# Performance work log

Measured on AMD Instinct MI355X. Metric: run time of the kernel, lower is better.

Reference implementation:

```python
import jax, jax.numpy as jnp
import numpy as np
from jax import lax

B = 512
P_KEEP = 0.5  # base dropout keep probability (p=0.5)


def conv(x, w, b, pad):
    y = lax.conv_general_dilated(x, w, (1, 1), [(pad, pad), (pad, pad)],
                                 dimension_numbers=('NCHW', 'OIHW', 'NCHW'))
    return y + b[None, :, None, None]


def maxpool3s2(x):
    return lax.reduce_window(x, -jnp.inf, lax.max, (1, 1, 3, 3), (1, 1, 2, 2), 'VALID')


def eb_linear(p_out, a, W):
    # Excitation backprop through a linear layer (bias ignored).
    # p_out: [B, out] marginal winning probs at layer output
    # a:     [B, in]  (non-negative) activations at layer input
    # W:     [out, in]
    Wp = jnp.maximum(W, 0.0)
    z = a @ Wp.T                              # [B, out]
    s = jnp.where(z > 0, p_out / z, 0.0)      # [B, out]
    return a * (s @ Wp)                       # [B, in]


def setup_inputs() -> dict:
    key = jax.random.key(0)
    ks = jax.random.split(key, 16)

    def w(k, shape, fan_in):
        return (jax.random.normal(k, shape, jnp.float32) / np.sqrt(fan_in)).astype(jnp.float32)

    return {
        'x': jax.random.normal(ks[0], (B, 3, 32, 32), jnp.float32),
        'noise': jax.random.uniform(ks[1], (B, 2048), jnp.float32),
        'conv1_w': w(ks[2], (96, 3, 5, 5), 3 * 25),
        'conv1_b': jnp.zeros((96,), jnp.float32),
        'conv2_w': w(ks[3], (128, 96, 5, 5), 96 * 25),
        'conv2_b': jnp.zeros((128,), jnp.float32),
        'conv3_w': w(ks[4], (256, 128, 5, 5), 128 * 25),
        'conv3_b': jnp.zeros((256,), jnp.float32),
        'fc1_w': w(ks[5], (2048, 1024), 1024),
        'fc1_b': jnp.zeros((2048,), jnp.float32),
        'fc2_w': w(ks[6], (2048, 2048), 2048),
        'fc2_b': jnp.zeros((2048,), jnp.float32),
        'fc3_w': w(ks[7], (10, 2048), 2048),
        'fc3_b': jnp.zeros((10,), jnp.float32),
        'label': jax.random.randint(ks[8], (B,), 0, 10),
    }


def reference(x, noise, conv1_w, conv1_b, conv2_w, conv2_b, conv3_w, conv3_b,
              fc1_w, fc1_b, fc2_w, fc2_b, fc3_w, fc3_b, label):
    h1 = maxpool3s2(jax.nn.relu(conv(x, conv1_w, conv1_b, 1)))   # [B,96,14,14]
    h2 = maxpool3s2(jax.nn.relu(conv(h1, conv2_w, conv2_b, 2)))  # [B,128,6,6]
    h3 = maxpool3s2(jax.nn.relu(conv(h2, conv3_w, conv3_b, 2)))  # [B,256,2,2]
    h4 = h3.reshape(h3.shape[0], -1)                             # [B,1024]
    h5 = jax.nn.relu(h4 @ fc1_w.T + fc1_b)                       # [B,2048]

    # --- Excitation backprop through latterModel (fc2 -> relu -> fc3), batched ---
    h6_eb = jax.nn.relu(h5 @ fc2_w.T + fc2_b)                    # [B,2048]
    p_out = jax.nn.one_hot(label, 10, dtype=h5.dtype)            # [B,10]
    p_h6 = eb_linear(p_out, h6_eb, fc3_w)                        # [B,2048]
    pebs = eb_linear(p_h6, h5, fc2_w)                            # [B,2048]

    # --- Excitation Dropout mask ---
    N = pebs.shape[1]
    num = (1.0 - P_KEEP) * (N - 1) * pebs
    retain_p = 1.0 - num / (num + P_KEEP * (1.0 - pebs))         # [B,2048]
    mask = (noise < retain_p).astype(h5.dtype)
    h_ed = jnp.where(retain_p > 0, h5 * mask / retain_p, 0.0)

    h6 = jax.nn.relu(h_ed @ fc2_w.T + fc2_b)                     # [B,2048]
    return h6 @ fc3_w.T + fc3_b                                  # [B,10]
```

## Files before the change

### kernel.cpp

```cpp
#include <hip/hip_runtime.h>
#include <hip/hip_bf16.h>


typedef __attribute__((ext_vector_type(8))) short bf16x8;
typedef __attribute__((ext_vector_type(4))) float f32x4;

__device__ __forceinline__ void split_bf16(float x, ushort& h, ushort& l) {
    __hip_bfloat16 bh = __float2bfloat16(x);
    float fh = __bfloat162float(bh);
    __hip_bfloat16 bl = __float2bfloat16(x - fh);
    h = *(ushort*)&bh;
    l = *(ushort*)&bl;
}

__device__ __forceinline__ void split3_bf16(float x, ushort& a, ushort& b,
                                            ushort& c) {
    __hip_bfloat16 ba = __float2bfloat16(x);
    float fa = __bfloat162float(ba);
    float r = x - fa;
    __hip_bfloat16 bb = __float2bfloat16(r);
    float fb = __bfloat162float(bb);
    __hip_bfloat16 bc = __float2bfloat16(r - fb);
    a = *(ushort*)&ba;
    b = *(ushort*)&bb;
    c = *(ushort*)&bc;
}

__device__ __forceinline__ void gld_lds16(const void* g, void* l) {
    __builtin_amdgcn_global_load_lds(
        (const __attribute__((address_space(1))) unsigned int*)g,
        (__attribute__((address_space(3))) unsigned int*)l, 16, 0, 0);
}

__global__ void zero_k(float4* __restrict__ p, int n4) {
    int idx = blockIdx.x * 256 + threadIdx.x;
    int stride = gridDim.x * 256;
    float4 z = {0.f, 0.f, 0.f, 0.f};
    for (int i = idx; i < n4; i += stride) p[i] = z;
}

__global__ void transw_k(const float* __restrict__ in, float* __restrict__ out,
                         int OC, int K) {
    int idx = blockIdx.x * 256 + threadIdx.x;
    if (idx >= OC * K) return;
    int oc = idx / K, k = idx % K;
    out[k * OC + oc] = in[idx];
}

__global__ void splitw_k(const float* __restrict__ in, ushort* __restrict__ hi,
                         ushort* __restrict__ lo, int OC, int IC) {
    int idx = blockIdx.x * 256 + threadIdx.x;
    if (idx >= OC * IC * 25) return;
    int oc = idx / (IC * 25);
    int r = idx % (IC * 25);
    int ic = r / 25, tap = r % 25;
    float v = in[idx];
    ushort h, l;
    split_bf16(v, h, l);
    size_t k = (size_t)oc * IC * 25 + tap * IC + ic;
    hi[k] = h;
    lo[k] = l;
}

__global__ void splitw3_k(const float* __restrict__ in, ushort* __restrict__ out,
                          int off, int total) {
    int idx = blockIdx.x * 256 + threadIdx.x;
    if (idx >= total) return;
    ushort a, b, c;
    split3_bf16(in[idx], a, b, c);
    out[idx] = a;
    out[idx + off] = b;
    out[idx + 2 * off] = c;
}

__global__ __launch_bounds__(256) void splitw3t_relu_k(
        const float* __restrict__ in, ushort* __restrict__ out, int off) {
    __shared__ float tile[64][65];
    const int bx = blockIdx.x & 31, by = blockIdx.x >> 5;
    const int j = threadIdx.x & 63, i0 = threadIdx.x >> 6;
    for (int i = i0; i < 64; i += 4)
        tile[i][j] = in[(size_t)(by * 64 + i) * 2048 + bx * 64 + j];
    __syncthreads();
    for (int r = i0; r < 64; r += 4) {
        float x = fmaxf(tile[j][r], 0.f);
        ushort a, b, c;
        split3_bf16(x, a, b, c);
        size_t o = (size_t)(bx * 64 + r) * 2048 + by * 64 + j;
        out[o] = a;
        out[o + off] = b;
        out[o + 2 * off] = c;
    }
}

__global__ __launch_bounds__(256) void conv1_v3(
        const float* __restrict__ x, const float* __restrict__ w1t,
        const float* __restrict__ b1, ushort* __restrict__ h1hi,
        ushort* __restrict__ h1lo) {
    __shared__ float simg[3 * 34 * 34];
    __shared__ float c1s[8][904];
    const int b = blockIdx.x, oc0 = blockIdx.y * 8, t = threadIdx.x;

    for (int i = t; i < 3 * 34 * 34; i += 256) simg[i] = 0.f;
    __syncthreads();
    for (int i = t; i < 3072; i += 256) {
        int ic = i >> 10, r = (i >> 5) & 31, c = i & 31;
        simg[ic * 1156 + (r + 1) * 34 + (c + 1)] = x[(size_t)b * 3072 + i];
    }
    __syncthreads();

    int base[4];
    bool valid[4];
#pragma unroll
    for (int j = 0; j < 4; j++) {
        int p = t + j * 256;
        valid[j] = p < 900;
        int oh = p / 30, ow = p % 30;
        base[j] = valid[j] ? oh * 34 + ow : 0;
    }

    float acc[4][8];
#pragma unroll
    for (int j = 0; j < 4; j++)
#pragma unroll
        for (int u = 0; u < 8; u++) acc[j][u] = 0.f;

#pragma unroll 1
    for (int ic = 0; ic < 3; ic++) {
        const int icb = ic * 1156;
#pragma unroll 1
        for (int kh = 0; kh < 5; kh++) {
#pragma unroll
            for (int kw = 0; kw < 5; kw++) {
                const float4* wr =
                    (const float4*)&w1t[(ic * 25 + kh * 5 + kw) * 96 + oc0];
                float4 w0 = wr[0], w1v = wr[1];
#pragma unroll
                for (int j = 0; j < 4; j++) {
                    float v = simg[icb + base[j] + kh * 34 + kw];
#pragma unroll
                    for (int u = 0; u < 4; u++) {
                        acc[j][u] = fmaf((&w0.x)[u], v, acc[j][u]);
                        acc[j][u + 4] = fmaf((&w1v.x)[u], v, acc[j][u + 4]);
                    }
                }
            }
        }
    }
#pragma unroll
    for (int j = 0; j < 4; j++)
        if (valid[j]) {
            int p = t + j * 256;
#pragma unroll
            for (int u = 0; u < 8; u++) c1s[u][p] = acc[j][u];
        }
    __syncthreads();
    if (t < 196) {
        const int ph = t / 14, pw = t % 14;
        ushort hv[8], lv[8];
#pragma unroll
        for (int u = 0; u < 8; u++) {
            float m = c1s[u][(2 * ph) * 30 + 2 * pw];
#pragma unroll
            for (int q = 1; q < 9; q++) {
                int dy = q / 3, dx = q % 3;
                m = fmaxf(m, c1s[u][(2 * ph + dy) * 30 + 2 * pw + dx]);
            }
            float o = fmaxf(m + b1[oc0 + u], 0.f);
            split_bf16(o, hv[u], lv[u]);
        }
        size_t ob = (((size_t)b * 18 + ph + 2) * 18 + pw + 2) * 96 + oc0;
        *(bf16x8*)&h1hi[ob] = *(bf16x8*)&hv[0];
        *(bf16x8*)&h1lo[ob] = *(bf16x8*)&lv[0];
    }
}

template <int IC, int H, int W, int OH, int OW, int OC, int NM>
__global__ __launch_bounds__(512, 2) void convmfma8_k(
        const ushort* __restrict__ ah, int aoff,
        const ushort* __restrict__ wh, int boff,
        const float* __restrict__ bias, float* __restrict__ C) {
    constexpr int K = 25 * IC;
    constexpr int G = NM * (OC / 128);
    __shared__ ushort At[2][128 * 64];
    __shared__ ushort Bt[2][128 * 64];
    const int t = threadIdx.x;
    const int lane = t & 63, wv = t >> 6;
    const int id = blockIdx.x;
    const int id2 = (id & 7) * (G >> 3) + (id >> 3);
    const int n0 = (id2 / NM) * 128;
    const int m0 = (id2 % NM) * 128;
    const int wm = (wv >> 1) * 32;
    const int wn = (wv & 1) * 64;

    const int srow = lane >> 3;
    const int slot = lane & 7;
    const int part = slot ^ srow;
    const bool hiA = part < 4;
    const int pk = (part & 3) * 8;

    int arb[2];
#pragma unroll
    for (int rr = 0; rr < 2; rr++) {
        int r = wv * 16 + rr * 8 + srow;
        int m = m0 + r;
        int b = m / (OH * OW), pxy = m % (OH * OW);
        int oh = pxy / OW, ow = pxy % OW;
        arb[rr] = ((b * H + oh) * W + ow) * IC + pk;
    }
    const ushort* __restrict__ aptr = ah + (hiA ? 0 : aoff);
    size_t brb[2];
#pragma unroll
    for (int rr = 0; rr < 2; rr++) {
        int r = wv * 16 + rr * 8 + srow;
        brb[rr] = (size_t)(n0 + r) * K + pk;
    }
    const ushort* __restrict__ bptr = wh + (hiA ? 0 : boff);

    f32x4 acc[2][4];
#pragma unroll
    for (int i = 0; i < 2; i++)
#pragma unroll
        for (int j = 0; j < 4; j++) acc[i][j] = (f32x4)(0.f);

    const int q = lane >> 4;
    const int fr = lane & 15;

    auto stage = [&](int buf, int k0s) {
        const int tap = k0s / IC;
        const int koff = ((tap / 5) * W + (tap % 5)) * IC + (k0s - tap * IC);
#pragma unroll
        for (int rr = 0; rr < 2; rr++)
            gld_lds16(aptr + arb[rr] + koff, &At[buf][(wv * 16 + rr * 8) * 64]);
#pragma unroll
        for (int rr = 0; rr < 2; rr++)
            gld_lds16(bptr + brb[rr] + k0s, &Bt[buf][(wv * 16 + rr * 8) * 64]);
    };

    stage(0, 0);
    __syncthreads();

    int cur = 0;
#pragma unroll 1
    for (int k0 = 0; k0 < K; k0 += 32) {
        bf16x8 afh[2], afl[2], bfh[4], bfl[4];
#pragma unroll
        for (int i = 0; i < 2; i++) {
            int row = wm + fr + i * 16;
            afh[i] = *(const bf16x8*)&At[cur][row * 64 + ((q ^ (row & 7)) << 3)];
            afl[i] = *(const bf16x8*)&At[cur][row * 64 + (((4 | q) ^ (row & 7)) << 3)];
        }
#pragma unroll
        for (int j = 0; j < 4; j++) {
            int row = wn + fr + j * 16;
            bfh[j] = *(const bf16x8*)&Bt[cur][row * 64 + ((q ^ (row & 7)) << 3)];
            bfl[j] = *(const bf16x8*)&Bt[cur][row * 64 + (((4 | q) ^ (row & 7)) << 3)];
        }
        const int nxt = k0 + 32;
        if (nxt < K) stage(cur ^ 1, nxt);

        __builtin_amdgcn_s_setprio(1);
#pragma unroll
        for (int i = 0; i < 2; i++)
#pragma unroll
            for (int j = 0; j < 4; j++) {
                acc[i][j] = __builtin_amdgcn_mfma_f32_16x16x32_bf16(
                    afh[i], bfh[j], acc[i][j], 0, 0, 0);
                acc[i][j] = __builtin_amdgcn_mfma_f32_16x16x32_bf16(
                    afh[i], bfl[j], acc[i][j], 0, 0, 0);
                acc[i][j] = __builtin_amdgcn_mfma_f32_16x16x32_bf16(
                    afl[i], bfh[j], acc[i][j], 0, 0, 0);
            }
        __builtin_amdgcn_s_setprio(0);
        __syncthreads();
        cur ^= 1;
    }

    const int crow0 = (lane >> 4) * 4;
    const int ccol = lane & 15;
#pragma unroll
    for (int i = 0; i < 2; i++) {
        int gm = m0 + wm + i * 16 + crow0;
#pragma unroll
        for (int j = 0; j < 4; j++) {
            int gn = n0 + wn + j * 16 + ccol;
            float bb = bias[gn];
#pragma unroll
            for (int r = 0; r < 4; r++)
                C[(size_t)(gm + r) * OC + gn] = acc[i][j][r] + bb;
        }
    }
}

template <int IC, int H, int W, int OH, int OW, int OC, int NM>
__global__ __launch_bounds__(256, 3) void convmfma9_k(
        const ushort* __restrict__ ah, int aoff,
        const ushort* __restrict__ wh, int boff,
        const float* __restrict__ bias, float* __restrict__ C) {
    constexpr int K = 25 * IC;
    constexpr int G = NM * (OC / 128);
    __shared__ ushort At[2][64 * 64];
    __shared__ ushort Bt[128 * 64];
    const int t = threadIdx.x;
    const int lane = t & 63, wv = t >> 6;
    const int id = blockIdx.x;
    const int id2 = (id & 7) * (G >> 3) + (id >> 3);
    const int n0 = (id2 / NM) * 128;
    const int m0 = (id2 % NM) * 64;
    const int wm = (wv >> 1) * 32;
    const int wn = (wv & 1) * 64;

    const int srow = lane >> 3;
    const int slot = lane & 7;
    const int part = slot ^ srow;
    const bool hiA = part < 4;
    const int pk = (part & 3) * 8;

    int arb[2];
#pragma unroll
    for (int rr = 0; rr < 2; rr++) {
        int r = wv * 16 + rr * 8 + srow;
        int m = m0 + r;
        int b = m / (OH * OW), pxy = m % (OH * OW);
        int oh = pxy / OW, ow = pxy % OW;
        arb[rr] = ((b * H + oh) * W + ow) * IC + pk;
    }
    const ushort* __restrict__ aptr = ah + (hiA ? 0 : aoff);
    size_t brb[4];
#pragma unroll
    for (int rr = 0; rr < 4; rr++) {
        int r = wv * 32 + rr * 8 + srow;
        brb[rr] = (size_t)(n0 + r) * K + pk;
    }
    const ushort* __restrict__ bptr = wh + (hiA ? 0 : boff);

    f32x4 acc[2][4];
#pragma unroll
    for (int i = 0; i < 2; i++)
#pragma unroll
        for (int j = 0; j < 4; j++) acc[i][j] = (f32x4)(0.f);

    const int q = lane >> 4;
    const int fr = lane & 15;

    auto stageA = [&](int buf, int k0s) {
        const int tap = k0s / IC;
        const int koff = ((tap / 5) * W + (tap % 5)) * IC + (k0s - tap * IC);
#pragma unroll
        for (int rr = 0; rr < 2; rr++)
            gld_lds16(aptr + arb[rr] + koff, &At[buf][(wv * 16 + rr * 8) * 64]);
    };
    auto stageB = [&](int k0s) {
#pragma unroll
        for (int rr = 0; rr < 4; rr++)
            gld_lds16(bptr + brb[rr] + k0s, &Bt[(wv * 32 + rr * 8) * 64]);
    };

    stageA(0, 0);
    stageB(0);
    __syncthreads();

    int cur = 0;
#pragma unroll 1
    for (int k0 = 0; k0 < K; k0 += 32) {
        bf16x8 bfh[4], bfl[4];
#pragma unroll
        for (int j = 0; j < 4; j++) {
            int row = wn + fr + j * 16;
            bfh[j] = *(const bf16x8*)&Bt[row * 64 + ((q ^ (row & 7)) << 3)];
            bfl[j] = *(const bf16x8*)&Bt[row * 64 + (((4 | q) ^ (row & 7)) << 3)];
        }
        __syncthreads();
        const int nxt = k0 + 32;
        if (nxt < K) {
            stageA(cur ^ 1, nxt);
            stageB(nxt);
        }
        bf16x8 afh[2], afl[2];
#pragma unroll
        for (int i = 0; i < 2; i++) {
            int row = wm + fr + i * 16;
            afh[i] = *(const bf16x8*)&At[cur][row * 64 + ((q ^ (row & 7)) << 3)];
            afl[i] = *(const bf16x8*)&At[cur][row * 64 + (((4 | q) ^ (row & 7)) << 3)];
        }
        __builtin_amdgcn_s_setprio(1);
#pragma unroll
        for (int i = 0; i < 2; i++)
#pragma unroll
            for (int j = 0; j < 4; j++) {
                acc[i][j] = __builtin_amdgcn_mfma_f32_16x16x32_bf16(
                    afh[i], bfh[j], acc[i][j], 0, 0, 0);
                acc[i][j] = __builtin_amdgcn_mfma_f32_16x16x32_bf16(
                    afh[i], bfl[j], acc[i][j], 0, 0, 0);
                acc[i][j] = __builtin_amdgcn_mfma_f32_16x16x32_bf16(
                    afl[i], bfh[j], acc[i][j], 0, 0, 0);
            }
        __builtin_amdgcn_s_setprio(0);
        __syncthreads();
        cur ^= 1;
    }

    const int crow0 = (lane >> 4) * 4;
    const int ccol = lane & 15;
#pragma unroll
    for (int i = 0; i < 2; i++) {
        int gm = m0 + wm + i * 16 + crow0;
#pragma unroll
        for (int j = 0; j < 4; j++) {
            int gn = n0 + wn + j * 16 + ccol;
            float bb = bias[gn];
#pragma unroll
            for (int r = 0; r < 4; r++)
                C[(size_t)(gm + r) * OC + gn] = acc[i][j][r] + bb;
        }
    }
}

__global__ void pool2_k(const float* __restrict__ in, ushort* __restrict__ ohi,
                        ushort* __restrict__ olo) {
    int idx = blockIdx.x * 256 + threadIdx.x;
    if (idx >= 512 * 36 * 128) return;
    int c = idx & 127;
    int tmp = idx >> 7;
    int pw = tmp % 6;
    int tmp2 = tmp / 6;
    int ph = tmp2 % 6;
    int b = tmp2 / 6;
    size_t base = (((size_t)b * 14 + 2 * ph) * 14 + 2 * pw) * 128 + c;
    float m = -3.4e38f;
#pragma unroll
    for (int dy = 0; dy < 3; dy++)
#pragma unroll
        for (int dx = 0; dx < 3; dx++)
            m = fmaxf(m, in[base + (dy * 14 + dx) * 128]);
    float v = fmaxf(m, 0.f);
    ushort h, l;
    split_bf16(v, h, l);
    size_t o = (((size_t)b * 10 + ph + 2) * 10 + pw + 2) * 128 + c;
    ohi[o] = h;
    olo[o] = l;
}

__global__ void pool3_k(const float* __restrict__ in, float* __restrict__ h3) {
    int idx = blockIdx.x * 256 + threadIdx.x;
    if (idx >= 512 * 4 * 256) return;
    int c = idx & 255;
    int pw = (idx >> 8) & 1;
    int ph = (idx >> 9) & 1;
    int b = idx >> 10;
    size_t base = (((size_t)b * 6 + 2 * ph) * 6 + 2 * pw) * 256 + c;
    float m = -3.4e38f;
#pragma unroll
    for (int dy = 0; dy < 3; dy++)
#pragma unroll
        for (int dx = 0; dx < 3; dx++)
            m = fmaxf(m, in[base + (dy * 6 + dx) * 256]);
    h3[(size_t)b * 1024 + c * 4 + ph * 2 + pw] = fmaxf(m, 0.f);
}

template <int BIAS, int RELUOUT, int DUAL>
__global__ __launch_bounds__(256, 4) void gemmfc_k(
        const float* __restrict__ A, const ushort* __restrict__ B3, int boff,
        const float* __restrict__ bias, float* __restrict__ C,
        float* __restrict__ C2, int K, int N) {
    __shared__ ushort Aa[32][44], Ab[32][44], Ac[32][44];
    __shared__ ushort Ba[64][44], Bb[64][44], Bc[64][44];
    const int t = threadIdx.x;
    const int n0 = blockIdx.x * 64;
    const int m0 = blockIdx.y * 32;
    const int lane = t & 63, wv = t >> 6;
    const int wm = (wv >> 1) * 16, wn = (wv & 1) * 32;
    const int fr = lane & 15, kp = (lane >> 4) * 8;

    f32x4 acc[2], acc2[DUAL ? 2 : 1];
#pragma unroll
    for (int j = 0; j < 2; j++) acc[j] = (f32x4)(0.f);
    if constexpr (DUAL) {
#pragma unroll
        for (int j = 0; j < 2; j++) acc2[j] = (f32x4)(0.f);
    }

    const int ar = t >> 2, ak = (t & 3) * 8;

    for (int k0 = 0; k0 < K; k0 += 32) {
        float4 a0, a1;
        if (t < 128) {
            a0 = *(const float4*)&A[(size_t)(m0 + ar) * K + k0 + ak];
            a1 = *(const float4*)&A[(size_t)(m0 + ar) * K + k0 + ak + 4];
        }
        size_t bidx = (size_t)(n0 + ar) * K + k0 + ak;
        bf16x8 b0 = *(const bf16x8*)&B3[bidx];
        bf16x8 b1 = *(const bf16x8*)&B3[bidx + boff];
        bf16x8 b2 = *(const bf16x8*)&B3[bidx + 2 * (size_t)boff];
        __syncthreads();
        if (t < 128) {
            ushort sa[8], sb[8], sc[8];
#pragma unroll
            for (int e = 0; e < 4; e++)
                split3_bf16((&a0.x)[e], sa[e], sb[e], sc[e]);
#pragma unroll
            for (int e = 0; e < 4; e++)
                split3_bf16((&a1.x)[e], sa[4 + e], sb[4 + e], sc[4 + e]);
            *(bf16x8*)&Aa[ar][ak] = *(bf16x8*)sa;
            *(bf16x8*)&Ab[ar][ak] = *(bf16x8*)sb;
            *(bf16x8*)&Ac[ar][ak] = *(bf16x8*)sc;
        }
        *(bf16x8*)&Ba[ar][ak] = b0;
        *(bf16x8*)&Bb[ar][ak] = b1;
        *(bf16x8*)&Bc[ar][ak] = b2;
        __syncthreads();

        bf16x8 fa = *(const bf16x8*)&Aa[wm + fr][kp];
        bf16x8 fb = *(const bf16x8*)&Ab[wm + fr][kp];
        bf16x8 fc = *(const bf16x8*)&Ac[wm + fr][kp];
#pragma unroll
        for (int j = 0; j < 2; j++) {
            int row = wn + j * 16 + fr;
            bf16x8 ga = *(const bf16x8*)&Ba[row][kp];
            bf16x8 gb = *(const bf16x8*)&Bb[row][kp];
            bf16x8 gc = *(const bf16x8*)&Bc[row][kp];
            acc[j] = __builtin_amdgcn_mfma_f32_16x16x32_bf16(fa, ga, acc[j], 0, 0, 0);
            acc[j] = __builtin_amdgcn_mfma_f32_16x16x32_bf16(fa, gb, acc[j], 0, 0, 0);
            acc[j] = __builtin_amdgcn_mfma_f32_16x16x32_bf16(fb, ga, acc[j], 0, 0, 0);
            acc[j] = __builtin_amdgcn_mfma_f32_16x16x32_bf16(fa, gc, acc[j], 0, 0, 0);
            acc[j] = __builtin_amdgcn_mfma_f32_16x16x32_bf16(fc, ga, acc[j], 0, 0, 0);
            acc[j] = __builtin_amdgcn_mfma_f32_16x16x32_bf16(fb, gb, acc[j], 0, 0, 0);
            if constexpr (DUAL) {
                bf16x8 msk = ga >> 15;
                bf16x8 ra = ga & ~msk;
                bf16x8 rb = gb & ~msk;
                bf16x8 rc = gc & ~msk;
                acc2[j] = __builtin_amdgcn_mfma_f32_16x16x32_bf16(fa, ra, acc2[j], 0, 0, 0);
                acc2[j] = __builtin_amdgcn_mfma_f32_16x16x32_bf16(fa, rb, acc2[j], 0, 0, 0);
                acc2[j] = __builtin_amdgcn_mfma_f32_16x16x32_bf16(fb, ra, acc2[j], 0, 0, 0);
                acc2[j] = __builtin_amdgcn_mfma_f32_16x16x32_bf16(fa, rc, acc2[j], 0, 0, 0);
                acc2[j] = __builtin_amdgcn_mfma_f32_16x16x32_bf16(fc, ra, acc2[j], 0, 0, 0);
                acc2[j] = __builtin_amdgcn_mfma_f32_16x16x32_bf16(fb, rb, acc2[j], 0, 0, 0);
            }
        }
    }

    const int gm0 = m0 + wm + (lane >> 4) * 4;
#pragma unroll
    for (int j = 0; j < 2; j++) {
        int gn = n0 + wn + j * 16 + fr;
        float bb = BIAS ? bias[gn] : 0.f;
#pragma unroll
        for (int r = 0; r < 4; r++) {
            float v = acc[j][r] + bb;
            if constexpr (RELUOUT) v = fmaxf(v, 0.f);
            C[(size_t)(gm0 + r) * N + gn] = v;
            if constexpr (DUAL) C2[(size_t)(gm0 + r) * N + gn] = acc2[j][r];
        }
    }
}

__global__ __launch_bounds__(256) void zlab_k(
        const float* __restrict__ h6eb, const float* __restrict__ w3,
        const int* __restrict__ label, float* __restrict__ zlab) {
    __shared__ float red[4];
    const int b = blockIdx.x, t = threadIdx.x;
    const int lab = label[b];
    const float4* hp = (const float4*)(h6eb + (size_t)b * 2048);
    const float4* wp = (const float4*)(w3 + (size_t)lab * 2048);
    float s = 0.f;
    for (int i = t; i < 512; i += 256) {
        float4 h = hp[i], w = wp[i];
        s += h.x * fmaxf(w.x, 0.f) + h.y * fmaxf(w.y, 0.f) +
             h.z * fmaxf(w.z, 0.f) + h.w * fmaxf(w.w, 0.f);
    }
#pragma unroll
    for (int off = 32; off > 0; off >>= 1) s += __shfl_down(s, off, 64);
    if ((t & 63) == 0) red[t >> 6] = s;
    __syncthreads();
    if (t == 0) zlab[b] = red[0] + red[1] + red[2] + red[3];
}

__global__ void s2_k(const float* __restrict__ h6eb, const float* __restrict__ z2,
                     const float* __restrict__ w3, const int* __restrict__ label,
                     const float* __restrict__ zlab, float* __restrict__ s2) {
    int idx = blockIdx.x * 256 + threadIdx.x;
    int b = idx >> 11, j = idx & 2047;
    float zl = zlab[b], zv = z2[idx];
    float v = 0.f;
    if (zl > 0.f && zv > 0.f) {
        float wp = fmaxf(w3[(size_t)label[b] * 2048 + j], 0.f);
        v = h6eb[idx] * wp / (zl * zv);
    }
    s2[idx] = v;
}

__global__ void edrop_k(const float* __restrict__ h5, const float* __restrict__ t,
                        const float* __restrict__ noise, float* __restrict__ hed) {
    int idx = blockIdx.x * 256 + threadIdx.x;
    float pe = h5[idx] * t[idx];
    float num = 1023.5f * pe;
    float retain = 1.f - num / (num + 0.5f * (1.f - pe));
    float m = (noise[idx] < retain) ? 1.f : 0.f;
    hed[idx] = (retain > 0.f) ? h5[idx] * m / retain : 0.f;
}

__global__ void fc3_out_k(const float* __restrict__ h6, const float* __restrict__ w,
                          const float* __restrict__ bias, float* __restrict__ out) {
    int idx = blockIdx.x * 256 + threadIdx.x;
    if (idx >= 5120) return;
    int b = idx / 10, c = idx % 10;
    const float4* hp = (const float4*)(h6 + (size_t)b * 2048);
    const float4* wp = (const float4*)(w + (size_t)c * 2048);
    float s = 0.f;
    for (int i = 0; i < 512; i++) {
        float4 h = hp[i], ww = wp[i];
        s += h.x * ww.x + h.y * ww.y + h.z * ww.z + h.w * ww.w;
    }
    out[idx] = s + bias[c];
}

extern "C" void kernel_launch(void* const* d_in, const int* in_sizes, int n_in,
                              void* d_out, int out_size, void* d_ws, size_t ws_size,
                              hipStream_t stream) {
    const float* x       = (const float*)d_in[0];
    const float* noise   = (const float*)d_in[1];
    const float* conv1_w = (const float*)d_in[2];
    const float* conv1_b = (const float*)d_in[3];
    const float* conv2_w = (const float*)d_in[4];
    const float* conv2_b = (const float*)d_in[5];
    const float* conv3_w = (const float*)d_in[6];
    const float* conv3_b = (const float*)d_in[7];
    const float* fc1_w   = (const float*)d_in[8];
    const float* fc1_b   = (const float*)d_in[9];
    const float* fc2_w   = (const float*)d_in[10];
    const float* fc2_b   = (const float*)d_in[11];
    const float* fc3_w   = (const float*)d_in[12];
    const float* fc3_b   = (const float*)d_in[13];
    const int*   label   = (const int*)d_in[14];
    float* out = (float*)d_out;

    const size_t N_H1 = (size_t)512 * 18 * 18 * 96;
    const size_t N_C2 = (size_t)512 * 14 * 14 * 128;
    const size_t N_H2 = (size_t)512 * 10 * 10 * 128;
    const size_t N_H3 = (size_t)512 * 1024;

    float* ws = (float*)d_ws;
    ushort* h1hi = (ushort*)ws;
    ushort* h1lo = h1hi + N_H1;
    float* c3 = ws;
    float* c2 = ws + N_H1;
    float* h5   = c2;
    float* h6eb = c2 + 1 * 1048576;
    float* z2   = c2 + 2 * 1048576;
    float* s2   = c2 + 3 * 1048576;
    float* tb   = c2 + 4 * 1048576;
    float* hed  = c2 + 5 * 1048576;
    float* h6   = c2 + 6 * 1048576;
    float* zlab = c2 + 7 * 1048576;
    ushort* h2hi = (ushort*)(ws + N_H1 + N_C2);
    ushort* h2lo = h2hi + N_H2;
    float* h3  = ws + N_H1 + N_C2 + N_H2;
    float* w1t = h3 + N_H3;
    ushort* w2sh = (ushort*)(w1t + 7200);
    ushort* w2sl = w2sh + 307200;
    ushort* w3sh = w2sl + 307200;
    ushort* w3sl = w3sh + 819200;
    ushort* w23  = w3sl + 819200;
    ushort* w2rt = w23 + 3 * 4194304;
    ushort* w13  = w2rt + 3 * 4194304;

    transw_k<<<(75 * 96 + 255) / 256, 256, 0, stream>>>(conv1_w, w1t, 96, 75);
    splitw_k<<<(307200 + 255) / 256, 256, 0, stream>>>(conv2_w, w2sh, w2sl, 128, 96);
    splitw_k<<<(819200 + 255) / 256, 256, 0, stream>>>(conv3_w, w3sh, w3sl, 256, 128);
    splitw3_k<<<16384, 256, 0, stream>>>(fc2_w, w23, 4194304, 4194304);
    splitw3t_relu_k<<<1024, 256, 0, stream>>>(fc2_w, w2rt, 4194304);
    splitw3_k<<<8192, 256, 0, stream>>>(fc1_w, w13, 2097152, 2097152);

    zero_k<<<2048, 256, 0, stream>>>((float4*)h1hi, (int)(N_H1 / 4));
    zero_k<<<2048, 256, 0, stream>>>((float4*)h2hi, (int)(N_H2 / 4));

    conv1_v3<<<dim3(512, 12), 256, 0, stream>>>(x, w1t, conv1_b, h1hi, h1lo);
    convmfma8_k<96, 18, 18, 14, 14, 128, 784><<<784, 512, 0, stream>>>(
        h1hi, (int)N_H1, w2sh, 307200, conv2_b, c2);
    pool2_k<<<(512 * 36 * 128 + 255) / 256, 256, 0, stream>>>(c2, h2hi, h2lo);
    convmfma9_k<128, 10, 10, 6, 6, 256, 288><<<576, 256, 0, stream>>>(
        h2hi, (int)N_H2, w3sh, 819200, conv3_b, c3);
    pool3_k<<<(512 * 4 * 256 + 255) / 256, 256, 0, stream>>>(c3, h3);

    gemmfc_k<1, 1, 0><<<dim3(32, 16), 256, 0, stream>>>(
        h3, w13, 2097152, fc1_b, h5, nullptr, 1024, 2048);

    gemmfc_k<1, 1, 1><<<dim3(32, 16), 256, 0, stream>>>(
        h5, w23, 4194304, fc2_b, h6eb, z2, 2048, 2048);

    zlab_k<<<512, 256, 0, stream>>>(h6eb, fc3_w, label, zlab);
    s2_k<<<4096, 256, 0, stream>>>(h6eb, z2, fc3_w, label, zlab, s2);

    gemmfc_k<0, 0, 0><<<dim3(32, 16), 256, 0, stream>>>(
        s2, w2rt, 4194304, nullptr, tb, nullptr, 2048, 2048);

    edrop_k<<<4096, 256, 0, stream>>>(h5, tb, noise, hed);

    gemmfc_k<1, 1, 0><<<dim3(32, 16), 256, 0, stream>>>(
        hed, w23, 4194304, fc2_b, h6, nullptr, 2048, 2048);

    fc3_out_k<<<20, 256, 0, stream>>>(h6, fc3_w, fc3_b, out);
}
```

Measured before the change: 814.9 us.

## Pre-split FC activations into bf16x3 in producers, zero only conv padding borders

Producer kernels (pool3, fc1 epilogue, a fused zlab+s2 kernel, edrop) now emit activations already split into three bf16 planes, so the FC GEMMs load bf16 directly instead of re-splitting fp32 A tiles on every N-block. zlab and s2 are merged into one kernel, and edrop is vectorized. The full zeroing of the padded h1/h2 buffers is replaced by kernels that zero only the padding borders. In exchange, activation traffic grows to three 16-bit planes and more workspace is used.

```diff
diff --git a/kernel.cpp b/kernel.cpp
--- a/kernel.cpp
+++ b/kernel.cpp
@@ -32,11 +32,52 @@
         (__attribute__((address_space(3))) unsigned int*)l, 16, 0, 0);
 }
 
-__global__ void zero_k(float4* __restrict__ p, int n4) {
+__global__ void zeroborder1_k(ushort* __restrict__ base, int aoff) {
     int idx = blockIdx.x * 256 + threadIdx.x;
-    int stride = gridDim.x * 256;
-    float4 z = {0.f, 0.f, 0.f, 0.f};
-    for (int i = idx; i < n4; i += stride) p[i] = z;
+    if (idx >= 512 * 128) return;
+    int s = idx & 127, b = idx >> 7;
+    int r, c;
+    if (s < 72) {
+        int q = s / 18;
+        r = (q < 2) ? q : q + 14;
+        c = s % 18;
+    } else {
+        int s2 = s - 72;
+        r = 2 + (s2 >> 2);
+        int q = s2 & 3;
+        c = (q < 2) ? q : q + 14;
+    }
+    size_t o = (((size_t)b * 18 + r) * 18 + c) * 96;
+    bf16x8 z = (bf16x8)(short)0;
+#pragma unroll
+    for (int i = 0; i < 12; i++) {
+        *(bf16x8*)&base[o + i * 8] = z;
+        *(bf16x8*)&base[o + aoff + i * 8] = z;
+    }
+}
+
+__global__ void zeroborder2_k(ushort* __restrict__ base, int aoff) {
+    int idx = blockIdx.x * 256 + threadIdx.x;
+    if (idx >= 512 * 64) return;
+    int s = idx & 63, b = idx >> 6;
+    int r, c;
+    if (s < 40) {
+        int q = s / 10;
+        r = (q < 2) ? q : q + 6;
+        c = s % 10;
+    } else {
+        int s2 = s - 40;
+        r = 2 + (s2 >> 2);
+        int q = s2 & 3;
+        c = (q < 2) ? q : q + 6;
+    }
+    size_t o = (((size_t)b * 10 + r) * 10 + c) * 128;
+    bf16x8 z = (bf16x8)(short)0;
+#pragma unroll
+    for (int i = 0; i < 16; i++) {
+        *(bf16x8*)&base[o + i * 8] = z;
+        *(bf16x8*)&base[o + aoff + i * 8] = z;
+    }
 }
 
 __global__ void transw_k(const float* __restrict__ in, float* __restrict__ out,
@@ -440,7 +481,8 @@
     olo[o] = l;
 }
 
-__global__ void pool3_k(const float* __restrict__ in, float* __restrict__ h3) {
+__global__ void pool3_k(const float* __restrict__ in, ushort* __restrict__ h3s,
+                        int off) {
     int idx = blockIdx.x * 256 + threadIdx.x;
     if (idx >= 512 * 4 * 256) return;
     int c = idx & 255;
@@ -454,14 +496,22 @@
 #pragma unroll
         for (int dx = 0; dx < 3; dx++)
             m = fmaxf(m, in[base + (dy * 6 + dx) * 256]);
-    h3[(size_t)b * 1024 + c * 4 + ph * 2 + pw] = fmaxf(m, 0.f);
-}
-
-template <int BIAS, int RELUOUT, int DUAL>
-__global__ __launch_bounds__(256, 4) void gemmfc_k(
-        const float* __restrict__ A, const ushort* __restrict__ B3, int boff,
+    float v = fmaxf(m, 0.f);
+    ushort a, bb, cc;
+    split3_bf16(v, a, bb, cc);
+    size_t o = (size_t)b * 1024 + c * 4 + ph * 2 + pw;
+    h3s[o] = a;
+    h3s[o + off] = bb;
+    h3s[o + 2 * off] = cc;
+}
+
+template <int BIAS, int RELUOUT, int DUAL, int SPLITOUT>
+__global__ __launch_bounds__(256, 4) void gemmfc2_k(
+        const ushort* __restrict__ A3, int aoff,
+        const ushort* __restrict__ B3, int boff,
         const float* __restrict__ bias, float* __restrict__ C,
-        float* __restrict__ C2, int K, int N) {
+        float* __restrict__ C2, ushort* __restrict__ C3, int coff,
+        int K, int N) {
     __shared__ ushort Aa[32][44], Ab[32][44], Ac[32][44];
     __shared__ ushort Ba[64][44], Bb[64][44], Bc[64][44];
     const int t = threadIdx.x;
@@ -482,10 +532,12 @@
     const int ar = t >> 2, ak = (t & 3) * 8;
 
     for (int k0 = 0; k0 < K; k0 += 32) {
-        float4 a0, a1;
+        bf16x8 a0, a1, a2;
         if (t < 128) {
-            a0 = *(const float4*)&A[(size_t)(m0 + ar) * K + k0 + ak];
-            a1 = *(const float4*)&A[(size_t)(m0 + ar) * K + k0 + ak + 4];
+            size_t aidx = (size_t)(m0 + ar) * K + k0 + ak;
+            a0 = *(const bf16x8*)&A3[aidx];
+            a1 = *(const bf16x8*)&A3[aidx + aoff];
+            a2 = *(const bf16x8*)&A3[aidx + 2 * (size_t)aoff];
         }
         size_t bidx = (size_t)(n0 + ar) * K + k0 + ak;
         bf16x8 b0 = *(const bf16x8*)&B3[bidx];
@@ -493,16 +545,9 @@
         bf16x8 b2 = *(const bf16x8*)&B3[bidx + 2 * (size_t)boff];
         __syncthreads();
         if (t < 128) {
-            ushort sa[8], sb[8], sc[8];
-#pragma unroll
-            for (int e = 0; e < 4; e++)
-                split3_bf16((&a0.x)[e], sa[e], sb[e], sc[e]);
-#pragma unroll
-            for (int e = 0; e < 4; e++)
-                split3_bf16((&a1.x)[e], sa[4 + e], sb[4 + e], sc[4 + e]);
-            *(bf16x8*)&Aa[ar][ak] = *(bf16x8*)sa;
-            *(bf16x8*)&Ab[ar][ak] = *(bf16x8*)sb;
-            *(bf16x8*)&Ac[ar][ak] = *(bf16x8*)sc;
+            *(bf16x8*)&Aa[ar][ak] = a0;
+            *(bf16x8*)&Ab[ar][ak] = a1;
+            *(bf16x8*)&Ac[ar][ak] = a2;
         }
         *(bf16x8*)&Ba[ar][ak] = b0;
         *(bf16x8*)&Bb[ar][ak] = b1;
@@ -548,16 +593,26 @@
         for (int r = 0; r < 4; r++) {
             float v = acc[j][r] + bb;
             if constexpr (RELUOUT) v = fmaxf(v, 0.f);
-            C[(size_t)(gm0 + r) * N + gn] = v;
-            if constexpr (DUAL) C2[(size_t)(gm0 + r) * N + gn] = acc2[j][r];
-        }
-    }
-}
-
-__global__ __launch_bounds__(256) void zlab_k(
-        const float* __restrict__ h6eb, const float* __restrict__ w3,
-        const int* __restrict__ label, float* __restrict__ zlab) {
+            size_t oidx = (size_t)(gm0 + r) * N + gn;
+            C[oidx] = v;
+            if constexpr (DUAL) C2[oidx] = acc2[j][r];
+            if constexpr (SPLITOUT) {
+                ushort sa, sb, sc;
+                split3_bf16(v, sa, sb, sc);
+                C3[oidx] = sa;
+                C3[oidx + coff] = sb;
+                C3[oidx + 2 * (size_t)coff] = sc;
+            }
+        }
+    }
+}
+
+__global__ __launch_bounds__(256) void zlab_s2_k(
+        const float* __restrict__ h6eb, const float* __restrict__ z2,
+        const float* __restrict__ w3, const int* __restrict__ label,
+        ushort* __restrict__ s2s, int soff) {
     __shared__ float red[4];
+    __shared__ float zls;
     const int b = blockIdx.x, t = threadIdx.x;
     const int lab = label[b];
     const float4* hp = (const float4*)(h6eb + (size_t)b * 2048);
@@ -572,31 +627,49 @@
     for (int off = 32; off > 0; off >>= 1) s += __shfl_down(s, off, 64);
     if ((t & 63) == 0) red[t >> 6] = s;
     __syncthreads();
-    if (t == 0) zlab[b] = red[0] + red[1] + red[2] + red[3];
-}
-
-__global__ void s2_k(const float* __restrict__ h6eb, const float* __restrict__ z2,
-                     const float* __restrict__ w3, const int* __restrict__ label,
-                     const float* __restrict__ zlab, float* __restrict__ s2) {
-    int idx = blockIdx.x * 256 + threadIdx.x;
-    int b = idx >> 11, j = idx & 2047;
-    float zl = zlab[b], zv = z2[idx];
-    float v = 0.f;
-    if (zl > 0.f && zv > 0.f) {
-        float wp = fmaxf(w3[(size_t)label[b] * 2048 + j], 0.f);
-        v = h6eb[idx] * wp / (zl * zv);
-    }
-    s2[idx] = v;
-}
-
-__global__ void edrop_k(const float* __restrict__ h5, const float* __restrict__ t,
-                        const float* __restrict__ noise, float* __restrict__ hed) {
-    int idx = blockIdx.x * 256 + threadIdx.x;
-    float pe = h5[idx] * t[idx];
-    float num = 1023.5f * pe;
-    float retain = 1.f - num / (num + 0.5f * (1.f - pe));
-    float m = (noise[idx] < retain) ? 1.f : 0.f;
-    hed[idx] = (retain > 0.f) ? h5[idx] * m / retain : 0.f;
+    if (t == 0) zls = red[0] + red[1] + red[2] + red[3];
+    __syncthreads();
+    const float zl = zls;
+
+    const float* hr = h6eb + (size_t)b * 2048;
+    const float* zr = z2 + (size_t)b * 2048;
+    const float* wr = w3 + (size_t)lab * 2048;
+    const int j0 = t * 8;
+    ushort va[8], vb[8], vc[8];
+#pragma unroll
+    for (int e = 0; e < 8; e++) {
+        int j = j0 + e;
+        float zv = zr[j];
+        float v = 0.f;
+        if (zl > 0.f && zv > 0.f) v = hr[j] * fmaxf(wr[j], 0.f) / (zl * zv);
+        split3_bf16(v, va[e], vb[e], vc[e]);
+    }
+    size_t o = (size_t)b * 2048 + j0;
+    *(bf16x8*)&s2s[o] = *(bf16x8*)va;
+    *(bf16x8*)&s2s[o + soff] = *(bf16x8*)vb;
+    *(bf16x8*)&s2s[o + 2 * (size_t)soff] = *(bf16x8*)vc;
+}
+
+__global__ void edrop_k(const float* __restrict__ h5, const float* __restrict__ tb,
+                        const float* __restrict__ noise, ushort* __restrict__ heds,
+                        int off) {
+    int i4 = (blockIdx.x * 256 + threadIdx.x) * 4;
+    float4 h = *(const float4*)&h5[i4];
+    float4 tt = *(const float4*)&tb[i4];
+    float4 nz = *(const float4*)&noise[i4];
+    ushort a[4], b[4], c[4];
+#pragma unroll
+    for (int e = 0; e < 4; e++) {
+        float pe = (&h.x)[e] * (&tt.x)[e];
+        float num = 1023.5f * pe;
+        float retain = 1.f - num / (num + 0.5f * (1.f - pe));
+        float m = ((&nz.x)[e] < retain) ? 1.f : 0.f;
+        float v = (retain > 0.f) ? (&h.x)[e] * m / retain : 0.f;
+        split3_bf16(v, a[e], b[e], c[e]);
+    }
+    *(ushort4*)&heds[i4] = *(ushort4*)a;
+    *(ushort4*)&heds[i4 + off] = *(ushort4*)b;
+    *(ushort4*)&heds[i4 + 2 * off] = *(ushort4*)c;
 }
 
 __global__ void fc3_out_k(const float* __restrict__ h6, const float* __restrict__ w,
@@ -637,7 +710,6 @@
     const size_t N_H1 = (size_t)512 * 18 * 18 * 96;
     const size_t N_C2 = (size_t)512 * 14 * 14 * 128;
     const size_t N_H2 = (size_t)512 * 10 * 10 * 128;
-    const size_t N_H3 = (size_t)512 * 1024;
 
     float* ws = (float*)d_ws;
     ushort* h1hi = (ushort*)ws;
@@ -647,15 +719,11 @@
     float* h5   = c2;
     float* h6eb = c2 + 1 * 1048576;
     float* z2   = c2 + 2 * 1048576;
-    float* s2   = c2 + 3 * 1048576;
-    float* tb   = c2 + 4 * 1048576;
-    float* hed  = c2 + 5 * 1048576;
-    float* h6   = c2 + 6 * 1048576;
-    float* zlab = c2 + 7 * 1048576;
+    float* tb   = c2 + 3 * 1048576;
+    float* h6   = c2 + 4 * 1048576;
     ushort* h2hi = (ushort*)(ws + N_H1 + N_C2);
     ushort* h2lo = h2hi + N_H2;
-    float* h3  = ws + N_H1 + N_C2 + N_H2;
-    float* w1t = h3 + N_H3;
+    float* w1t = ws + N_H1 + N_C2 + N_H2;
     ushort* w2sh = (ushort*)(w1t + 7200);
     ushort* w2sl = w2sh + 307200;
     ushort* w3sh = w2sl + 307200;
@@ -663,6 +731,10 @@
     ushort* w23  = w3sl + 819200;
     ushort* w2rt = w23 + 3 * 4194304;
     ushort* w13  = w2rt + 3 * 4194304;
+    ushort* h3s3 = w13 + 3 * 2097152;
+    ushort* h5s3 = h3s3 + 3 * 524288;
+    ushort* s2s3 = h5s3 + 3 * 1048576;
+    ushort* heds3 = s2s3 + 3 * 1048576;
 
     transw_k<<<(75 * 96 + 255) / 256, 256, 0, stream>>>(conv1_w, w1t, 96, 75);
     splitw_k<<<(307200 + 255) / 256, 256, 0, stream>>>(conv2_w, w2sh, w2sl, 128, 96);
@@ -671,8 +743,8 @@
     splitw3t_relu_k<<<1024, 256, 0, stream>>>(fc2_w, w2rt, 4194304);
     splitw3_k<<<8192, 256, 0, stream>>>(fc1_w, w13, 2097152, 2097152);
 
-    zero_k<<<2048, 256, 0, stream>>>((float4*)h1hi, (int)(N_H1 / 4));
-    zero_k<<<2048, 256, 0, stream>>>((float4*)h2hi, (int)(N_H2 / 4));
+    zeroborder1_k<<<256, 256, 0, stream>>>(h1hi, (int)N_H1);
+    zeroborder2_k<<<128, 256, 0, stream>>>(h2hi, (int)N_H2);
 
     conv1_v3<<<dim3(512, 12), 256, 0, stream>>>(x, w1t, conv1_b, h1hi, h1lo);
     convmfma8_k<96, 18, 18, 14, 14, 128, 784><<<784, 512, 0, stream>>>(
@@ -680,24 +752,27 @@
     pool2_k<<<(512 * 36 * 128 + 255) / 256, 256, 0, stream>>>(c2, h2hi, h2lo);
     convmfma9_k<128, 10, 10, 6, 6, 256, 288><<<576, 256, 0, stream>>>(
         h2hi, (int)N_H2, w3sh, 819200, conv3_b, c3);
-    pool3_k<<<(512 * 4 * 256 + 255) / 256, 256, 0, stream>>>(c3, h3);
-
-    gemmfc_k<1, 1, 0><<<dim3(32, 16), 256, 0, stream>>>(
-        h3, w13, 2097152, fc1_b, h5, nullptr, 1024, 2048);
-
-    gemmfc_k<1, 1, 1><<<dim3(32, 16), 256, 0, stream>>>(
-        h5, w23, 4194304, fc2_b, h6eb, z2, 2048, 2048);
-
-    zlab_k<<<512, 256, 0, stream>>>(h6eb, fc3_w, label, zlab);
-    s2_k<<<4096, 256, 0, stream>>>(h6eb, z2, fc3_w, label, zlab, s2);
-
-    gemmfc_k<0, 0, 0><<<dim3(32, 16), 256, 0, stream>>>(
-        s2, w2rt, 4194304, nullptr, tb, nullptr, 2048, 2048);
-
-    edrop_k<<<4096, 256, 0, stream>>>(h5, tb, noise, hed);
-
-    gemmfc_k<1, 1, 0><<<dim3(32, 16), 256, 0, stream>>>(
-        hed, w23, 4194304, fc2_b, h6, nullptr, 2048, 2048);
+    pool3_k<<<(512 * 4 * 256 + 255) / 256, 256, 0, stream>>>(c3, h3s3, 524288);
+
+    gemmfc2_k<1, 1, 0, 1><<<dim3(32, 16), 256, 0, stream>>>(
+        h3s3, 524288, w13, 2097152, fc1_b, h5, nullptr, h5s3, 1048576,
+        1024, 2048);
+
+    gemmfc2_k<1, 1, 1, 0><<<dim3(32, 16), 256, 0, stream>>>(
+        h5s3, 1048576, w23, 4194304, fc2_b, h6eb, z2, nullptr, 0,
+        2048, 2048);
+
+    zlab_s2_k<<<512, 256, 0, stream>>>(h6eb, z2, fc3_w, label, s2s3, 1048576);
+
+    gemmfc2_k<0, 0, 0, 0><<<dim3(32, 16), 256, 0, stream>>>(
+        s2s3, 1048576, w2rt, 4194304, nullptr, tb, nullptr, nullptr, 0,
+        2048, 2048);
+
+    edrop_k<<<1024, 256, 0, stream>>>(h5, tb, noise, heds3, 1048576);
+
+    gemmfc2_k<1, 1, 0, 0><<<dim3(32, 16), 256, 0, stream>>>(
+        heds3, 1048576, w23, 4194304, fc2_b, h6, nullptr, nullptr, 0,
+        2048, 2048);
 
     fc3_out_k<<<20, 256, 0, stream>>>(h6, fc3_w, fc3_b, out);
 }
```

Result: no change. 818.5 us (median of 2 runs) (+0.4%).
